# Optimization experiments

Hardware: AMD Instinct MI355X
Metric: run time of the kernel (lower is better)

Reference implementation:

```python
import jax, jax.numpy as jnp
import numpy as np

D_K = 64
N_HEADS = 16
D_MODEL = 1024
EPS = 1e-5


def setup_inputs() -> dict:
    key = jax.random.key(0)
    ks = jax.random.split(key, 8)
    B, S = 2, 2048
    scale = 1.0 / np.sqrt(D_MODEL)
    inp = {
        "input_Q": jax.random.normal(ks[0], (B, S, D_MODEL), jnp.float32),
        "input_K": jax.random.normal(ks[1], (B, S, D_MODEL), jnp.float32),
        "input_V": jax.random.normal(ks[2], (B, S, D_MODEL), jnp.float32),
        "attn_mask": jax.random.randint(ks[3], (B, S, S), 0, 2) == 1,
        "W_Q": jax.random.normal(ks[4], (D_MODEL, N_HEADS * D_K), jnp.float32) * scale,
        "W_K": jax.random.normal(ks[5], (D_MODEL, N_HEADS * D_K), jnp.float32) * scale,
        "W_V": jax.random.normal(ks[6], (D_MODEL, N_HEADS * D_K), jnp.float32) * scale,
        "W_fc": jax.random.normal(ks[7], (N_HEADS * D_K, D_MODEL), jnp.float32) * scale,
    }
    return inp


def _layer_norm(x):
    mu = jnp.mean(x, axis=-1, keepdims=True)
    var = jnp.var(x, axis=-1, keepdims=True)
    return (x - mu) / jnp.sqrt(var + EPS)


def reference(input_Q, input_K, input_V, attn_mask, W_Q, W_K, W_V, W_fc):
    B, S, _ = input_Q.shape
    # projections -> [B, H, S, d_k]
    Q = (input_Q @ W_Q).reshape(B, S, N_HEADS, D_K).transpose(0, 2, 1, 3)
    K = (input_K @ W_K).reshape(B, S, N_HEADS, D_K).transpose(0, 2, 1, 3)
    V = (input_V @ W_V).reshape(B, S, N_HEADS, D_K).transpose(0, 2, 1, 3)
    scores = jnp.einsum("bhqd,bhkd->bhqk", Q, K) / np.sqrt(D_K)
    scores = jnp.where(attn_mask[:, None, :, :], -1e9, scores)
    attn = jax.nn.softmax(scores, axis=-1)
    context = jnp.einsum("bhqk,bhkd->bhqd", attn, V)
    context = context.transpose(0, 2, 1, 3).reshape(B, S, N_HEADS * D_K)
    output = context @ W_fc
    return _layer_norm(output + input_Q), attn
```

## Files before the change

### kernel.cpp

```cpp
#include <hip/hip_runtime.h>

typedef __bf16 bf16x8 __attribute__((ext_vector_type(8)));
typedef unsigned short u16x8 __attribute__((ext_vector_type(8)));
typedef unsigned short u16x4 __attribute__((ext_vector_type(4)));
typedef float f32x4 __attribute__((ext_vector_type(4)));

#define DEV static __device__ __forceinline__

DEV unsigned short f2bf(float f) {
  union { float f; unsigned u; } v; v.f = f;
  unsigned u = v.u + 0x7FFFu + ((v.u >> 16) & 1u);
  return (unsigned short)(u >> 16);
}

DEV unsigned short f2bf_hw(float f) {
  union { __bf16 b; unsigned short u; } v;
  v.b = (__bf16)f;
  return v.u;
}

DEV float bf2f(unsigned short b) {
  union { unsigned u; float f; } v; v.u = ((unsigned)b) << 16;
  return v.f;
}

DEV float fast_exp2(float x) { return __builtin_amdgcn_exp2f(x); }

DEV int swz(int row, int k) { return row * 64 + (k ^ ((row & 7) * 8)); }

DEV int swzV(int row, int k) {
  return row * 64 + (k ^ ((row & 7) * 8) ^ (((row >> 3) & 7) * 8));
}

#define GLOAD16(gp, lp)                                                        \
  __builtin_amdgcn_global_load_lds(                                            \
      (const __attribute__((address_space(1))) void*)(const void*)(gp),        \
      (__attribute__((address_space(3))) void*)(void*)(lp), 16, 0, 0)

__global__ __launch_bounds__(256) void k_detect(const unsigned* m, int* flag) {
  __shared__ int sF, sI;
  if (threadIdx.x == 0) { sF = 1; sI = 1; }
  __syncthreads();
  int lF = 1, lI = 1;
  for (int i = threadIdx.x; i < 4096; i += 256) {
    unsigned d = m[i];
    lF &= (d == 0u || d == 0x3F800000u);
    lI &= (d == 0u || d == 1u);
  }
  if (!lF) atomicAnd(&sF, 0);
  if (!lI) atomicAnd(&sI, 0);
  __syncthreads();
  if (threadIdx.x == 0) flag[0] = sF ? 2 : (sI ? 0 : 1);
}

__global__ __launch_bounds__(256) void k_pack(const void* m, const int* flag,
                                              unsigned long long* bits) {
  const int tid = threadIdx.x;
  const int w = blockIdx.x * 4 + (tid >> 6);
  const int lane = tid & 63;
  const size_t idx = (size_t)w * 64 + lane;
  const int fl = flag[0];
  int v;
  if (fl == 1)      v = ((const unsigned char*)m)[idx];
  else if (fl == 0) v = ((const int*)m)[idx];
  else              v = (((const float*)m)[idx] != 0.f);
  unsigned long long bal = __ballot(v != 0);
  if (lane == 0) bits[w] = bal;
}

__global__ __launch_bounds__(256) void k_cvt(const float* a, const float* b,
                                             const float* c, unsigned short* out) {
  const int gid = blockIdx.x * 256 + threadIdx.x;
  const int which = gid >> 20;
  const int loc = gid & 1048575;
  const float* src = which == 0 ? a : which == 1 ? b : c;
  float4 f = ((const float4*)src)[loc];
  ushort4 u = make_ushort4(f2bf(f.x), f2bf(f.y), f2bf(f.z), f2bf(f.w));
  *(ushort4*)(out + (size_t)which * 4194304 + (size_t)loc * 4) = u;
}

__global__ __launch_bounds__(256) void k_wt(const float* w0, const float* w1,
                                            const float* w2, const float* w3,
                                            unsigned short* out) {
  __shared__ float t[32][33];
  const int z = blockIdx.z;
  const float* W = z == 0 ? w0 : z == 1 ? w1 : z == 2 ? w2 : w3;
  unsigned short* Wt = out + (size_t)z * 1048576;
  const int x = threadIdx.x, y = threadIdx.y;
  const int k0 = blockIdx.x * 32, n0 = blockIdx.y * 32;
#pragma unroll
  for (int r = 0; r < 4; ++r)
    t[y + r * 8][x] = W[(size_t)(k0 + y + r * 8) * 1024 + n0 + x];
  __syncthreads();
#pragma unroll
  for (int r = 0; r < 4; ++r)
    Wt[(size_t)(n0 + y + r * 8) * 1024 + k0 + x] = f2bf(t[x][y + r * 8]);
}

__global__ __launch_bounds__(256) void k_gemm(
    const unsigned short* __restrict__ A0, const unsigned short* __restrict__ A1,
    const unsigned short* __restrict__ A2, const unsigned short* __restrict__ B0,
    const unsigned short* __restrict__ B1, const unsigned short* __restrict__ B2,
    unsigned short* __restrict__ C0, unsigned short* __restrict__ C1,
    unsigned short* __restrict__ C2, float* __restrict__ Cf) {
  __shared__ __align__(16) unsigned short As[128 * 64];
  __shared__ __align__(16) unsigned short Bs[128 * 64];
  const int z = blockIdx.z;
  const unsigned short* A = z == 0 ? A0 : z == 1 ? A1 : A2;
  const unsigned short* Bt = z == 0 ? B0 : z == 1 ? B1 : B2;
  unsigned short* Cb = z == 0 ? C0 : z == 1 ? C1 : C2;

  const int tid = threadIdx.x, lane = tid & 63, wid = tid >> 6;
  const int mt = blockIdx.x, nt = blockIdx.y;
  const int wm = (wid >> 1) * 64, wn = (wid & 1) * 64;
  const int lr = lane >> 3;
  const int lc = ((lane & 7) ^ (lane >> 3)) * 8;
  const int l15 = lane & 15, lg = lane >> 4;
  f32x4 acc[4][4] = {};

  for (int kt = 0; kt < 16; ++kt) {
    const int k0 = kt * 64;
#pragma unroll
    for (int c = wid; c < 16; c += 4) {
      GLOAD16(A + (size_t)(mt * 128 + c * 8 + lr) * 1024 + k0 + lc, As + c * 512);
      GLOAD16(Bt + (size_t)(nt * 128 + c * 8 + lr) * 1024 + k0 + lc, Bs + c * 512);
    }
    __syncthreads();
#pragma unroll
    for (int ks = 0; ks < 2; ++ks) {
      const int ko = ks * 32 + lg * 8;
      bf16x8 af[4], bfr[4];
#pragma unroll
      for (int f = 0; f < 4; ++f) {
        af[f] = *(const bf16x8*)(As + swz(wm + f * 16 + l15, ko));
        bfr[f] = *(const bf16x8*)(Bs + swz(wn + f * 16 + l15, ko));
      }
#pragma unroll
      for (int i = 0; i < 4; ++i)
#pragma unroll
        for (int j = 0; j < 4; ++j)
          acc[i][j] = __builtin_amdgcn_mfma_f32_16x16x32_bf16(af[i], bfr[j],
                                                              acc[i][j], 0, 0, 0);
    }
    __syncthreads();
  }
  const int rbase = mt * 128 + wm + lg * 4;
  const int cbase = nt * 128 + wn + l15;
#pragma unroll
  for (int i = 0; i < 4; ++i)
#pragma unroll
    for (int j = 0; j < 4; ++j) {
      const int col = cbase + j * 16;
#pragma unroll
      for (int r = 0; r < 4; ++r) {
        const int row = rbase + i * 16 + r;
        if (Cf) Cf[(size_t)row * 1024 + col] = acc[i][j][r];
        else    Cb[(size_t)row * 1024 + col] = f2bf(acc[i][j][r]);
      }
    }
}

__global__ __launch_bounds__(256) void k_attn(
    const unsigned short* __restrict__ PQ, const unsigned short* __restrict__ PK,
    const unsigned short* __restrict__ PV_, const unsigned long long* __restrict__ bits,
    float* __restrict__ attn_out, unsigned short* __restrict__ CTX) {
  __shared__ __align__(16) unsigned short KB[2][64 * 64];
  __shared__ __align__(16) unsigned short VB[2][64 * 64];
  __shared__ __align__(16) unsigned short Ps[4][16 * 64];

  const int tid = threadIdx.x, lane = tid & 63, wid = tid >> 6;
  const int qt = blockIdx.x, h = blockIdx.y, b = blockIdx.z;
  const int q0 = qt * 64;
  const int lr = lane >> 3;
  const int lc = ((lane & 7) ^ (lane >> 3)) * 8;
  const int l15 = lane & 15, lg = lane >> 4;
  const size_t rowK = (size_t)(b * 2048) * 1024 + h * 64;
  const float C = 0.125f * 1.44269504f;

#pragma unroll
  for (int c = wid; c < 8; c += 4)
    GLOAD16(PQ + rowK + (size_t)(q0 + c * 8 + lr) * 1024 + lc, KB[0] + c * 512);
  __syncthreads();
  const bf16x8 qf0 = *(const bf16x8*)(KB[0] + swz(wid * 16 + l15, lg * 8));
  const bf16x8 qf1 = *(const bf16x8*)(KB[0] + swz(wid * 16 + l15, 32 + lg * 8));
  const unsigned long long* mrow =
      bits + (size_t)(b * 2048 + q0 + wid * 16 + lg * 4) * 32;
  __syncthreads();

#pragma unroll
  for (int c = wid; c < 8; c += 4)
    GLOAD16(PK + rowK + (size_t)(c * 8 + lr) * 1024 + lc, KB[0] + c * 512);
  __syncthreads();

  float rs[4] = {0.f, 0.f, 0.f, 0.f};
  int cur = 0;
  for (int kt = 0; kt < 32; ++kt) {
    if (kt < 31) {
#pragma unroll
      for (int c = wid; c < 8; c += 4)
        GLOAD16(PK + rowK + (size_t)((kt + 1) * 64 + c * 8 + lr) * 1024 + lc,
                KB[cur ^ 1] + c * 512);
    }
    const unsigned long long w0 = mrow[kt], w1 = mrow[32 + kt],
                             w2 = mrow[64 + kt], w3 = mrow[96 + kt];
#pragma unroll
    for (int fn = 0; fn < 4; ++fn) {
      const bf16x8 kf0 = *(const bf16x8*)(KB[cur] + swz(fn * 16 + l15, lg * 8));
      const bf16x8 kf1 = *(const bf16x8*)(KB[cur] + swz(fn * 16 + l15, 32 + lg * 8));
      f32x4 s = {};
      s = __builtin_amdgcn_mfma_f32_16x16x32_bf16(qf0, kf0, s, 0, 0, 0);
      s = __builtin_amdgcn_mfma_f32_16x16x32_bf16(qf1, kf1, s, 0, 0, 0);
      const int kb = fn * 16 + l15;
      rs[0] += ((w0 >> kb) & 1) ? 0.f : fast_exp2(s[0] * C);
      rs[1] += ((w1 >> kb) & 1) ? 0.f : fast_exp2(s[1] * C);
      rs[2] += ((w2 >> kb) & 1) ? 0.f : fast_exp2(s[2] * C);
      rs[3] += ((w3 >> kb) & 1) ? 0.f : fast_exp2(s[3] * C);
    }
    __syncthreads();
    cur ^= 1;
  }
#pragma unroll
  for (int r = 0; r < 4; ++r) {
#pragma unroll
    for (int m = 1; m < 16; m <<= 1) rs[r] += __shfl_xor(rs[r], m);
    rs[r] = 1.f / rs[r];
  }

  const int vr = tid >> 3, d0 = (tid & 7) * 8;
  {
#pragma unroll
    for (int c = wid; c < 8; c += 4)
      GLOAD16(PK + rowK + (size_t)(c * 8 + lr) * 1024 + lc, KB[0] + c * 512);
    u16x8 v0 = *(const u16x8*)(PV_ + rowK + (size_t)vr * 1024 + d0);
    u16x8 v1 = *(const u16x8*)(PV_ + rowK + (size_t)(32 + vr) * 1024 + d0);
#pragma unroll
    for (int e = 0; e < 8; ++e) VB[0][swzV(d0 + e, vr)] = v0[e];
#pragma unroll
    for (int e = 0; e < 8; ++e) VB[0][swzV(d0 + e, 32 + vr)] = v1[e];
    __syncthreads();
  }

  f32x4 cacc[4] = {};
  cur = 0;
  const int srow = lane >> 2, scg = lane & 3;
  float* arow = attn_out + ((size_t)(b * 16 + h) * 2048 + q0 + wid * 16 + srow) * 2048;
  for (int kt = 0; kt < 32; ++kt) {
    const int k0 = kt * 64;
    u16x8 nv0, nv1;
    if (kt < 31) {
      const size_t nb = rowK + (size_t)((kt + 1) * 64) * 1024;
      nv0 = *(const u16x8*)(PV_ + nb + (size_t)vr * 1024 + d0);
      nv1 = *(const u16x8*)(PV_ + nb + (size_t)(32 + vr) * 1024 + d0);
#pragma unroll
      for (int c = wid; c < 8; c += 4)
        GLOAD16(PK + nb + (size_t)(c * 8 + lr) * 1024 + lc, KB[cur ^ 1] + c * 512);
    }
    const unsigned long long wm_[4] = {mrow[kt], mrow[32 + kt], mrow[64 + kt],
                                       mrow[96 + kt]};
#pragma unroll
    for (int fn = 0; fn < 4; ++fn) {
      const bf16x8 kf0 = *(const bf16x8*)(KB[cur] + swz(fn * 16 + l15, lg * 8));
      const bf16x8 kf1 = *(const bf16x8*)(KB[cur] + swz(fn * 16 + l15, 32 + lg * 8));
      f32x4 s = {};
      s = __builtin_amdgcn_mfma_f32_16x16x32_bf16(qf0, kf0, s, 0, 0, 0);
      s = __builtin_amdgcn_mfma_f32_16x16x32_bf16(qf1, kf1, s, 0, 0, 0);
      const int kb = fn * 16 + l15;
#pragma unroll
      for (int r = 0; r < 4; ++r) {
        const float p =
            ((wm_[r] >> kb) & 1) ? 0.f : fast_exp2(s[r] * C) * rs[r];
        Ps[wid][swz(lg * 4 + r, kb)] = f2bf_hw(p);
      }
    }
#pragma unroll
    for (int j = 0; j < 4; ++j) {
      const int c = scg * 4 + j * 16;
      const u16x4 pb = *(const u16x4*)(&Ps[wid][swz(srow, c)]);
      float4 o;
      o.x = bf2f(pb[0]); o.y = bf2f(pb[1]); o.z = bf2f(pb[2]); o.w = bf2f(pb[3]);
      *(float4*)(arow + k0 + c) = o;
    }
#pragma unroll
    for (int ks = 0; ks < 2; ++ks) {
      const int ko = ks * 32 + lg * 8;
      const bf16x8 pf = *(const bf16x8*)(&Ps[wid][swz(l15, ko)]);
#pragma unroll
      for (int fn = 0; fn < 4; ++fn) {
        const bf16x8 vf = *(const bf16x8*)(VB[cur] + swzV(fn * 16 + l15, ko));
        cacc[fn] = __builtin_amdgcn_mfma_f32_16x16x32_bf16(pf, vf, cacc[fn], 0, 0, 0);
      }
    }
    if (kt < 31) {
#pragma unroll
      for (int e = 0; e < 8; ++e) VB[cur ^ 1][swzV(d0 + e, vr)] = nv0[e];
#pragma unroll
      for (int e = 0; e < 8; ++e) VB[cur ^ 1][swzV(d0 + e, 32 + vr)] = nv1[e];
    }
    __syncthreads();
    cur ^= 1;
  }
#pragma unroll
  for (int fn = 0; fn < 4; ++fn)
#pragma unroll
    for (int r = 0; r < 4; ++r) {
      const int q = q0 + wid * 16 + lg * 4 + r;
      CTX[(size_t)(b * 2048 + q) * 1024 + h * 64 + fn * 16 + l15] =
          f2bf_hw(cacc[fn][r]);
    }
}

__global__ __launch_bounds__(256) void k_ln(const float* __restrict__ PRE,
                                            const float* __restrict__ inQ,
                                            float* __restrict__ out) {
  const int row = blockIdx.x, tid = threadIdx.x;
  const size_t base = (size_t)row * 1024 + tid * 4;
  const float4 x = *(const float4*)(PRE + base);
  const float4 q = *(const float4*)(inQ + base);
  const float v0 = x.x + q.x, v1 = x.y + q.y, v2 = x.z + q.z, v3 = x.w + q.w;
  float s = v0 + v1 + v2 + v3;
  float ss = v0 * v0 + v1 * v1 + v2 * v2 + v3 * v3;
#pragma unroll
  for (int m = 1; m < 64; m <<= 1) {
    s += __shfl_xor(s, m);
    ss += __shfl_xor(ss, m);
  }
  __shared__ float red[8];
  const int wid = tid >> 6, lane = tid & 63;
  if (lane == 0) { red[wid] = s; red[4 + wid] = ss; }
  __syncthreads();
  if (tid == 0) {
    const float S = red[0] + red[1] + red[2] + red[3];
    const float SS = red[4] + red[5] + red[6] + red[7];
    const float mu = S * (1.f / 1024.f);
    const float var = SS * (1.f / 1024.f) - mu * mu;
    red[0] = mu;
    red[1] = rsqrtf(var + 1e-5f);
  }
  __syncthreads();
  const float mu = red[0], rstd = red[1];
  float4 o;
  o.x = (v0 - mu) * rstd; o.y = (v1 - mu) * rstd;
  o.z = (v2 - mu) * rstd; o.w = (v3 - mu) * rstd;
  *(float4*)(out + base) = o;
}

extern "C" void kernel_launch(void* const* d_in, const int* in_sizes, int n_in,
                              void* d_out, int out_size, void* d_ws, size_t ws_size,
                              hipStream_t stream) {
  const float* inQ = (const float*)d_in[0];
  const float* inK = (const float*)d_in[1];
  const float* inV = (const float*)d_in[2];
  const void* msk = d_in[3];
  const float* wq = (const float*)d_in[4];
  const float* wk = (const float*)d_in[5];
  const float* wv = (const float*)d_in[6];
  const float* wf = (const float*)d_in[7];

  char* ws = (char*)d_ws;
  unsigned short* XQ = (unsigned short*)(ws);
  unsigned short* WT = (unsigned short*)(ws + 25165824);
  unsigned short* PQ = (unsigned short*)(ws + 33554432);
  unsigned short* PK = (unsigned short*)(ws + 41943040);
  unsigned short* PV = (unsigned short*)(ws + 50331648);
  unsigned short* CTX = (unsigned short*)(ws + 58720256);
  float* PRE = (float*)(ws + 67108864);
  unsigned long long* BITS = (unsigned long long*)(ws + 83886080);
  int* FLAG = (int*)(ws + 84934656);

  float* outLN = (float*)d_out;
  float* outAT = (float*)d_out + 4194304;

  k_detect<<<1, 256, 0, stream>>>((const unsigned*)msk, FLAG);
  k_pack<<<32768, 256, 0, stream>>>(msk, FLAG, BITS);
  k_cvt<<<12288, 256, 0, stream>>>(inQ, inK, inV, XQ);
  k_wt<<<dim3(32, 32, 4), dim3(32, 8, 1), 0, stream>>>(wq, wk, wv, wf, WT);
  k_gemm<<<dim3(32, 8, 3), 256, 0, stream>>>(XQ, XQ + 4194304, XQ + 8388608,
                                             WT, WT + 1048576, WT + 2097152,
                                             PQ, PK, PV, nullptr);
  k_attn<<<dim3(32, 16, 2), 256, 0, stream>>>(PQ, PK, PV, BITS, outAT, CTX);
  k_gemm<<<dim3(32, 8, 1), 256, 0, stream>>>(CTX, CTX, CTX, WT + 3145728,
                                             WT + 3145728, WT + 3145728,
                                             nullptr, nullptr, nullptr, PRE);
  k_ln<<<4096, 256, 0, stream>>>(PRE, inQ, outLN);
}
```

Baseline: 395.2 us.

## Split attention into context pass and parallel attn-matrix writer kernel

The single attention kernel ran two full QK passes: one for row sums, then one writing the probability matrix and accumulating context. Now the first kernel computes unnormalized exp, row sums and P·V in one pass, normalizing the context at the end and storing reciprocal row sums. A second kernel recomputes QK over a quarter of the key range per block (4x more blocks) to write the normalized attention matrix. This drops the V work from the write pass and raises parallelism for the dominant attention-matrix store, at the cost of an extra launch and small RS buffer. The context now uses unnormalized bf16 probabilities, which changes rounding slightly.

```diff
diff --git a/kernel.cpp b/kernel.cpp
--- a/kernel.cpp
+++ b/kernel.cpp
@@ -160,10 +160,10 @@
     }
 }
 
-__global__ __launch_bounds__(256) void k_attn(
+__global__ __launch_bounds__(256) void k_attnA(
     const unsigned short* __restrict__ PQ, const unsigned short* __restrict__ PK,
     const unsigned short* __restrict__ PV_, const unsigned long long* __restrict__ bits,
-    float* __restrict__ attn_out, unsigned short* __restrict__ CTX) {
+    float* __restrict__ RS, unsigned short* __restrict__ CTX) {
   __shared__ __align__(16) unsigned short KB[2][64 * 64];
   __shared__ __align__(16) unsigned short VB[2][64 * 64];
   __shared__ __align__(16) unsigned short Ps[4][16 * 64];
@@ -187,22 +187,35 @@
       bits + (size_t)(b * 2048 + q0 + wid * 16 + lg * 4) * 32;
   __syncthreads();
 
-#pragma unroll
-  for (int c = wid; c < 8; c += 4)
-    GLOAD16(PK + rowK + (size_t)(c * 8 + lr) * 1024 + lc, KB[0] + c * 512);
-  __syncthreads();
+  const int vr = tid >> 3, d0 = (tid & 7) * 8;
+  {
+#pragma unroll
+    for (int c = wid; c < 8; c += 4)
+      GLOAD16(PK + rowK + (size_t)(c * 8 + lr) * 1024 + lc, KB[0] + c * 512);
+    u16x8 v0 = *(const u16x8*)(PV_ + rowK + (size_t)vr * 1024 + d0);
+    u16x8 v1 = *(const u16x8*)(PV_ + rowK + (size_t)(32 + vr) * 1024 + d0);
+#pragma unroll
+    for (int e = 0; e < 8; ++e) VB[0][swzV(d0 + e, vr)] = v0[e];
+#pragma unroll
+    for (int e = 0; e < 8; ++e) VB[0][swzV(d0 + e, 32 + vr)] = v1[e];
+    __syncthreads();
+  }
 
   float rs[4] = {0.f, 0.f, 0.f, 0.f};
+  f32x4 cacc[4] = {};
   int cur = 0;
   for (int kt = 0; kt < 32; ++kt) {
+    u16x8 nv0, nv1;
     if (kt < 31) {
+      const size_t nb = rowK + (size_t)((kt + 1) * 64) * 1024;
+      nv0 = *(const u16x8*)(PV_ + nb + (size_t)vr * 1024 + d0);
+      nv1 = *(const u16x8*)(PV_ + nb + (size_t)(32 + vr) * 1024 + d0);
 #pragma unroll
       for (int c = wid; c < 8; c += 4)
-        GLOAD16(PK + rowK + (size_t)((kt + 1) * 64 + c * 8 + lr) * 1024 + lc,
-                KB[cur ^ 1] + c * 512);
-    }
-    const unsigned long long w0 = mrow[kt], w1 = mrow[32 + kt],
-                             w2 = mrow[64 + kt], w3 = mrow[96 + kt];
+        GLOAD16(PK + nb + (size_t)(c * 8 + lr) * 1024 + lc, KB[cur ^ 1] + c * 512);
+    }
+    const unsigned long long wm_[4] = {mrow[kt], mrow[32 + kt], mrow[64 + kt],
+                                       mrow[96 + kt]};
 #pragma unroll
     for (int fn = 0; fn < 4; ++fn) {
       const bf16x8 kf0 = *(const bf16x8*)(KB[cur] + swz(fn * 16 + l15, lg * 8));
@@ -211,49 +224,103 @@
       s = __builtin_amdgcn_mfma_f32_16x16x32_bf16(qf0, kf0, s, 0, 0, 0);
       s = __builtin_amdgcn_mfma_f32_16x16x32_bf16(qf1, kf1, s, 0, 0, 0);
       const int kb = fn * 16 + l15;
-      rs[0] += ((w0 >> kb) & 1) ? 0.f : fast_exp2(s[0] * C);
-      rs[1] += ((w1 >> kb) & 1) ? 0.f : fast_exp2(s[1] * C);
-      rs[2] += ((w2 >> kb) & 1) ? 0.f : fast_exp2(s[2] * C);
-      rs[3] += ((w3 >> kb) & 1) ? 0.f : fast_exp2(s[3] * C);
+#pragma unroll
+      for (int r = 0; r < 4; ++r) {
+        const float p =
+            ((wm_[r] >> kb) & 1) ? 0.f : fast_exp2(s[r] * C);
+        rs[r] += p;
+        Ps[wid][swz(lg * 4 + r, kb)] = f2bf_hw(p);
+      }
+    }
+#pragma unroll
+    for (int ks = 0; ks < 2; ++ks) {
+      const int ko = ks * 32 + lg * 8;
+      const bf16x8 pf = *(const bf16x8*)(&Ps[wid][swz(l15, ko)]);
+#pragma unroll
+      for (int fn = 0; fn < 4; ++fn) {
+        const bf16x8 vf = *(const bf16x8*)(VB[cur] + swzV(fn * 16 + l15, ko));
+        cacc[fn] = __builtin_amdgcn_mfma_f32_16x16x32_bf16(pf, vf, cacc[fn], 0, 0, 0);
+      }
+    }
+    if (kt < 31) {
+#pragma unroll
+      for (int e = 0; e < 8; ++e) VB[cur ^ 1][swzV(d0 + e, vr)] = nv0[e];
+#pragma unroll
+      for (int e = 0; e < 8; ++e) VB[cur ^ 1][swzV(d0 + e, 32 + vr)] = nv1[e];
     }
     __syncthreads();
     cur ^= 1;
   }
+  float rsr[4];
 #pragma unroll
   for (int r = 0; r < 4; ++r) {
 #pragma unroll
     for (int m = 1; m < 16; m <<= 1) rs[r] += __shfl_xor(rs[r], m);
-    rs[r] = 1.f / rs[r];
-  }
-
-  const int vr = tid >> 3, d0 = (tid & 7) * 8;
-  {
-#pragma unroll
-    for (int c = wid; c < 8; c += 4)
-      GLOAD16(PK + rowK + (size_t)(c * 8 + lr) * 1024 + lc, KB[0] + c * 512);
-    u16x8 v0 = *(const u16x8*)(PV_ + rowK + (size_t)vr * 1024 + d0);
-    u16x8 v1 = *(const u16x8*)(PV_ + rowK + (size_t)(32 + vr) * 1024 + d0);
-#pragma unroll
-    for (int e = 0; e < 8; ++e) VB[0][swzV(d0 + e, vr)] = v0[e];
-#pragma unroll
-    for (int e = 0; e < 8; ++e) VB[0][swzV(d0 + e, 32 + vr)] = v1[e];
-    __syncthreads();
-  }
-
-  f32x4 cacc[4] = {};
-  cur = 0;
+    rsr[r] = 1.f / rs[r];
+  }
+#pragma unroll
+  for (int fn = 0; fn < 4; ++fn)
+#pragma unroll
+    for (int r = 0; r < 4; ++r) {
+      const int q = q0 + wid * 16 + lg * 4 + r;
+      CTX[(size_t)(b * 2048 + q) * 1024 + h * 64 + fn * 16 + l15] =
+          f2bf_hw(cacc[fn][r] * rsr[r]);
+    }
+  if (l15 == 0) {
+#pragma unroll
+    for (int r = 0; r < 4; ++r)
+      RS[(size_t)(b * 16 + h) * 2048 + q0 + wid * 16 + lg * 4 + r] = rsr[r];
+  }
+}
+
+__global__ __launch_bounds__(256) void k_attnC(
+    const unsigned short* __restrict__ PQ, const unsigned short* __restrict__ PK,
+    const unsigned long long* __restrict__ bits, const float* __restrict__ RS,
+    float* __restrict__ attn_out) {
+  __shared__ __align__(16) unsigned short KB[2][64 * 64];
+  __shared__ __align__(16) unsigned short Ps[4][16 * 64];
+
+  const int tid = threadIdx.x, lane = tid & 63, wid = tid >> 6;
+  const int qt = blockIdx.x, h = blockIdx.y;
+  const int b = blockIdx.z >> 2, kq = blockIdx.z & 3;
+  const int ktlo = kq * 8, kthi = ktlo + 8;
+  const int q0 = qt * 64;
+  const int lr = lane >> 3;
+  const int lc = ((lane & 7) ^ (lane >> 3)) * 8;
+  const int l15 = lane & 15, lg = lane >> 4;
+  const size_t rowK = (size_t)(b * 2048) * 1024 + h * 64;
+  const float C = 0.125f * 1.44269504f;
+
+#pragma unroll
+  for (int c = wid; c < 8; c += 4)
+    GLOAD16(PQ + rowK + (size_t)(q0 + c * 8 + lr) * 1024 + lc, KB[0] + c * 512);
+  __syncthreads();
+  const bf16x8 qf0 = *(const bf16x8*)(KB[0] + swz(wid * 16 + l15, lg * 8));
+  const bf16x8 qf1 = *(const bf16x8*)(KB[0] + swz(wid * 16 + l15, 32 + lg * 8));
+  const unsigned long long* mrow =
+      bits + (size_t)(b * 2048 + q0 + wid * 16 + lg * 4) * 32;
+  float rsr[4];
+#pragma unroll
+  for (int r = 0; r < 4; ++r)
+    rsr[r] = RS[(size_t)(b * 16 + h) * 2048 + q0 + wid * 16 + lg * 4 + r];
+  __syncthreads();
+
+#pragma unroll
+  for (int c = wid; c < 8; c += 4)
+    GLOAD16(PK + rowK + (size_t)(ktlo * 64 + c * 8 + lr) * 1024 + lc,
+            KB[0] + c * 512);
+  __syncthreads();
+
   const int srow = lane >> 2, scg = lane & 3;
   float* arow = attn_out + ((size_t)(b * 16 + h) * 2048 + q0 + wid * 16 + srow) * 2048;
-  for (int kt = 0; kt < 32; ++kt) {
+  int cur = 0;
+  for (int kt = ktlo; kt < kthi; ++kt) {
     const int k0 = kt * 64;
-    u16x8 nv0, nv1;
-    if (kt < 31) {
-      const size_t nb = rowK + (size_t)((kt + 1) * 64) * 1024;
-      nv0 = *(const u16x8*)(PV_ + nb + (size_t)vr * 1024 + d0);
-      nv1 = *(const u16x8*)(PV_ + nb + (size_t)(32 + vr) * 1024 + d0);
+    if (kt < kthi - 1) {
 #pragma unroll
       for (int c = wid; c < 8; c += 4)
-        GLOAD16(PK + nb + (size_t)(c * 8 + lr) * 1024 + lc, KB[cur ^ 1] + c * 512);
+        GLOAD16(PK + rowK + (size_t)((kt + 1) * 64 + c * 8 + lr) * 1024 + lc,
+                KB[cur ^ 1] + c * 512);
     }
     const unsigned long long wm_[4] = {mrow[kt], mrow[32 + kt], mrow[64 + kt],
                                        mrow[96 + kt]};
@@ -268,7 +335,7 @@
 #pragma unroll
       for (int r = 0; r < 4; ++r) {
         const float p =
-            ((wm_[r] >> kb) & 1) ? 0.f : fast_exp2(s[r] * C) * rs[r];
+            ((wm_[r] >> kb) & 1) ? 0.f : fast_exp2(s[r] * C) * rsr[r];
         Ps[wid][swz(lg * 4 + r, kb)] = f2bf_hw(p);
       }
     }
@@ -280,33 +347,9 @@
       o.x = bf2f(pb[0]); o.y = bf2f(pb[1]); o.z = bf2f(pb[2]); o.w = bf2f(pb[3]);
       *(float4*)(arow + k0 + c) = o;
     }
-#pragma unroll
-    for (int ks = 0; ks < 2; ++ks) {
-      const int ko = ks * 32 + lg * 8;
-      const bf16x8 pf = *(const bf16x8*)(&Ps[wid][swz(l15, ko)]);
-#pragma unroll
-      for (int fn = 0; fn < 4; ++fn) {
-        const bf16x8 vf = *(const bf16x8*)(VB[cur] + swzV(fn * 16 + l15, ko));
-        cacc[fn] = __builtin_amdgcn_mfma_f32_16x16x32_bf16(pf, vf, cacc[fn], 0, 0, 0);
-      }
-    }
-    if (kt < 31) {
-#pragma unroll
-      for (int e = 0; e < 8; ++e) VB[cur ^ 1][swzV(d0 + e, vr)] = nv0[e];
-#pragma unroll
-      for (int e = 0; e < 8; ++e) VB[cur ^ 1][swzV(d0 + e, 32 + vr)] = nv1[e];
-    }
     __syncthreads();
     cur ^= 1;
   }
-#pragma unroll
-  for (int fn = 0; fn < 4; ++fn)
-#pragma unroll
-    for (int r = 0; r < 4; ++r) {
-      const int q = q0 + wid * 16 + lg * 4 + r;
-      CTX[(size_t)(b * 2048 + q) * 1024 + h * 64 + fn * 16 + l15] =
-          f2bf_hw(cacc[fn][r]);
-    }
 }
 
 __global__ __launch_bounds__(256) void k_ln(const float* __restrict__ PRE,
@@ -365,7 +408,8 @@
   unsigned short* CTX = (unsigned short*)(ws + 58720256);
   float* PRE = (float*)(ws + 67108864);
   unsigned long long* BITS = (unsigned long long*)(ws + 83886080);
-  int* FLAG = (int*)(ws + 84934656);
+  float* RS = (float*)(ws + 84934656);
+  int* FLAG = (int*)(ws + 85196800);
 
   float* outLN = (float*)d_out;
   float* outAT = (float*)d_out + 4194304;
@@ -377,7 +421,8 @@
   k_gemm<<<dim3(32, 8, 3), 256, 0, stream>>>(XQ, XQ + 4194304, XQ + 8388608,
                                              WT, WT + 1048576, WT + 2097152,
                                              PQ, PK, PV, nullptr);
-  k_attn<<<dim3(32, 16, 2), 256, 0, stream>>>(PQ, PK, PV, BITS, outAT, CTX);
+  k_attnA<<<dim3(32, 16, 2), 256, 0, stream>>>(PQ, PK, PV, BITS, RS, CTX);
+  k_attnC<<<dim3(32, 16, 8), 256, 0, stream>>>(PQ, PK, BITS, RS, outAT);
   k_gemm<<<dim3(32, 8, 1), 256, 0, stream>>>(CTX, CTX, CTX, WT + 3145728,
                                              WT + 3145728, WT + 3145728,
                                              nullptr, nullptr, nullptr, PRE);
```

New measurement: 364.0 us (median of 2 runs). 1.09x faster.
